# Kernel tuning notes

Hardware: AMD Instinct MI355X
Metric: run time of the kernel (lower is better)

The kernel has to match this reference:

```python
import math
import jax, jax.numpy as jnp
import numpy as np

L = 16
T = 2 ** 19
F = 2
N_MIN = 16
N_MAX = 512
BOUND = 3.0
BATCH = 524288

_b = math.exp((math.log(N_MAX) - math.log(N_MIN)) / (L - 1))
NS = np.array([int(N_MIN * _b ** i) for i in range(L)], dtype=np.float32)  # resolutions per level
PRIMES = np.array([1, 2654435761, 805459861], dtype=np.uint32)
# 8 cube-corner offsets (x,y,z) in {0,1}
OFFSETS = np.array([[x, y, z] for x in (0, 1) for y in (0, 1) for z in (0, 1)], dtype=np.uint32)


def setup_inputs() -> dict:
    key = jax.random.key(0)
    k_pos, k_tab = jax.random.split(key)
    inputs = jax.random.uniform(k_pos, (BATCH, 3), dtype=jnp.float32, minval=-BOUND, maxval=BOUND)
    hash_table = jax.random.uniform(k_tab, (L, T, F), dtype=jnp.float32) * 0.0002 - 0.0001
    return {"inputs": inputs, "hash_table": hash_table}


def reference(inputs, hash_table):
    x = (inputs + BOUND) / (2 * BOUND)                      # [B,3] in [0,1]
    widths = jnp.asarray(1.0 / NS)[:, None, None]           # [L,1,1], width = 1/n per level
    pmin = jnp.floor(x[None] / widths)                      # [L,B,3] floor cell coord (== torch //)
    per = (x[None] - pmin * widths) / widths                # [L,B,3] fractional position in cell
    offs = jnp.asarray(OFFSETS)                             # [8,3] uint32
    corners = pmin.astype(jnp.uint32)[:, :, None, :] + offs[None, None]  # [L,B,8,3]
    prod = corners * jnp.asarray(PRIMES)                    # uint32 mul wraps mod 2^32
    idx = (prod[..., 0] ^ prod[..., 1] ^ prod[..., 2]) % jnp.uint32(T)   # [L,B,8]
    feats = jax.vmap(lambda tab, i: tab[i])(hash_table, idx)             # [L,B,8,F] gathers
    # trilinear weights: use per where offset bit is 1, (1-per) where 0
    w = jnp.prod(jnp.where(offs[None, None].astype(bool), per[:, :, None, :], 1.0 - per[:, :, None, :]), axis=-1)  # [L,B,8]
    feat = jnp.einsum('lbcf,lbc->lbf', feats, w)            # [L,B,F]
    B = inputs.shape[0]
    return feat.transpose(1, 0, 2).reshape(B, L * F)
```

## Files before the change

kernel.cpp:

```cpp
#include <hip/hip_runtime.h>
#include <cstdint>
#include <cstddef>


#define NUM_LEVELS 16
#define TBL_MASK ((1u << 19) - 1u)
#define PRIME_Y 2654435761u
#define PRIME_Z 805459861u
#define BATCH 524288

typedef float nfloat4 __attribute__((ext_vector_type(4)));
typedef double ndouble2 __attribute__((ext_vector_type(2)));

__constant__ float c_ns[NUM_LEVELS] = {
    16.f, 20.f, 25.f, 32.f, 40.f, 50.f, 64.f, 80.f,
    101.f, 128.f, 161.f, 203.f, 256.f, 322.f, 406.f, 512.f
};

__device__ __forceinline__ float2 d2f2(double d) {
    union { double d; float2 f; } u;
    u.d = d;
    return u.f;
}

__device__ __forceinline__ double f22d(float2 f) {
    union { double d; float2 f; } u;
    u.f = f;
    return u.d;
}

__global__ __launch_bounds__(256) void enc_level_kernel(
    const float* __restrict__ in,
    const float* __restrict__ table,
    double* __restrict__ ws,
    int base_level)
{
    const int slot = blockIdx.x & 7;
    const int chunk = blockIdx.x >> 3;
    const int l = base_level + slot;
    const int p = chunk * 256 + threadIdx.x;

    const float vx = __builtin_nontemporal_load(&in[p * 3 + 0]);
    const float vy = __builtin_nontemporal_load(&in[p * 3 + 1]);
    const float vz = __builtin_nontemporal_load(&in[p * 3 + 2]);
    const float xs = (vx + 3.0f) / 6.0f;
    const float ys = (vy + 3.0f) / 6.0f;
    const float zs = (vz + 3.0f) / 6.0f;

    const float n = c_ns[l];
    const float tx = xs * n, ty = ys * n, tz = zs * n;
    const float fpx = floorf(tx), fpy = floorf(ty), fpz = floorf(tz);
    const float wx1 = tx - fpx, wy1 = ty - fpy, wz1 = tz - fpz;
    const uint32_t px = (uint32_t)fpx;
    const uint32_t py = (uint32_t)fpy;
    const uint32_t pz = (uint32_t)fpz;

    const uint32_t hy0 = py * PRIME_Y, hy1 = hy0 + PRIME_Y;
    const uint32_t hz0 = pz * PRIME_Z, hz1 = hz0 + PRIME_Z;
    const uint32_t b0 = hy0 ^ hz0, b1 = hy0 ^ hz1;
    const uint32_t b2 = hy1 ^ hz0, b3 = hy1 ^ hz1;

    const uint32_t i00 = (px ^ b0) & TBL_MASK;
    const uint32_t i01 = (px ^ b1) & TBL_MASK;
    const uint32_t i02 = (px ^ b2) & TBL_MASK;
    const uint32_t i03 = (px ^ b3) & TBL_MASK;
    const uint32_t qx = px + 1u;
    const uint32_t i40 = (qx ^ b0) & TBL_MASK;
    const uint32_t i41 = (qx ^ b1) & TBL_MASK;
    const uint32_t i42 = (qx ^ b2) & TBL_MASK;
    const uint32_t i43 = (qx ^ b3) & TBL_MASK;

    const double* __restrict__ tb = ((const double*)table) + ((size_t)l << 19);
    const ndouble2* __restrict__ tb2 = (const ndouble2*)tb;

    const ndouble2 q0 = tb2[i00 >> 1];
    const ndouble2 q1 = tb2[i01 >> 1];
    const ndouble2 q2 = tb2[i02 >> 1];
    const ndouble2 q3 = tb2[i03 >> 1];

    const bool odd = (px & 1u) != 0u;
    double g0 = 0.0, g1 = 0.0, g2 = 0.0, g3 = 0.0;
    if (odd) {
        g0 = tb[i40];
        g1 = tb[i41];
        g2 = tb[i42];
        g3 = tb[i43];
    }

    const double e00 = (i00 & 1u) ? q0.y : q0.x;
    const double e01 = (i01 & 1u) ? q1.y : q1.x;
    const double e02 = (i02 & 1u) ? q2.y : q2.x;
    const double e03 = (i03 & 1u) ? q3.y : q3.x;
    const double p00 = (i00 & 1u) ? q0.x : q0.y;
    const double p01 = (i01 & 1u) ? q1.x : q1.y;
    const double p02 = (i02 & 1u) ? q2.x : q2.y;
    const double p03 = (i03 & 1u) ? q3.x : q3.y;

    float2 f[8];
    f[0] = d2f2(e00); f[1] = d2f2(e01); f[2] = d2f2(e02); f[3] = d2f2(e03);
    f[4] = d2f2(odd ? g0 : p00);
    f[5] = d2f2(odd ? g1 : p01);
    f[6] = d2f2(odd ? g2 : p02);
    f[7] = d2f2(odd ? g3 : p03);

    const float wx0 = 1.0f - wx1;
    const float wy0 = 1.0f - wy1;
    const float wz0 = 1.0f - wz1;

    float a0 = 0.0f, a1 = 0.0f, w;
    w = wx0 * wy0 * wz0; a0 = fmaf(f[0].x, w, a0); a1 = fmaf(f[0].y, w, a1);
    w = wx0 * wy0 * wz1; a0 = fmaf(f[1].x, w, a0); a1 = fmaf(f[1].y, w, a1);
    w = wx0 * wy1 * wz0; a0 = fmaf(f[2].x, w, a0); a1 = fmaf(f[2].y, w, a1);
    w = wx0 * wy1 * wz1; a0 = fmaf(f[3].x, w, a0); a1 = fmaf(f[3].y, w, a1);
    w = wx1 * wy0 * wz0; a0 = fmaf(f[4].x, w, a0); a1 = fmaf(f[4].y, w, a1);
    w = wx1 * wy0 * wz1; a0 = fmaf(f[5].x, w, a0); a1 = fmaf(f[5].y, w, a1);
    w = wx1 * wy1 * wz0; a0 = fmaf(f[6].x, w, a0); a1 = fmaf(f[6].y, w, a1);
    w = wx1 * wy1 * wz1; a0 = fmaf(f[7].x, w, a0); a1 = fmaf(f[7].y, w, a1);

    __builtin_nontemporal_store(f22d(make_float2(a0, a1)),
                                &ws[(size_t)l * BATCH + p]);
}

__global__ __launch_bounds__(256) void transpose_kernel(
    const double* __restrict__ ws,
    nfloat4* __restrict__ out)
{
    __shared__ double lds[256][NUM_LEVELS + 1];

    const int tid = threadIdx.x;
    const int p0 = blockIdx.x * 256;

#pragma unroll
    for (int l = 0; l < NUM_LEVELS; ++l) {
        lds[tid][l] = __builtin_nontemporal_load(&ws[(size_t)l * BATCH + p0 + tid]);
    }
    __syncthreads();

#pragma unroll
    for (int it = 0; it < 8; ++it) {
        const int e = it * 256 + tid;
        const int p = e >> 3;
        const int j = e & 7;
        const float2 a = d2f2(lds[p][2 * j]);
        const float2 b = d2f2(lds[p][2 * j + 1]);
        nfloat4 r;
        r.x = a.x; r.y = a.y; r.z = b.x; r.w = b.y;
        __builtin_nontemporal_store(r, &out[(size_t)blockIdx.x * 2048 + e]);
    }
}

struct Corner8 {
    uint32_t i[8];
    float wx0, wy0, wz0;
};

__device__ __forceinline__ Corner8 corner_setup_xyz(
    float xs, float ys, float zs, float n)
{
    const float tx = xs * n, ty = ys * n, tz = zs * n;
    const float fpx = floorf(tx), fpy = floorf(ty), fpz = floorf(tz);

    Corner8 c;
    c.wx0 = tx - fpx;
    c.wy0 = ty - fpy;
    c.wz0 = tz - fpz;

    const uint32_t px = (uint32_t)fpx;
    const uint32_t py = (uint32_t)fpy;
    const uint32_t pz = (uint32_t)fpz;

    const uint32_t hx0 = px;
    const uint32_t hx1 = px + 1u;
    const uint32_t hy0 = py * PRIME_Y;
    const uint32_t hy1 = hy0 + PRIME_Y;
    const uint32_t hz0 = pz * PRIME_Z;
    const uint32_t hz1 = hz0 + PRIME_Z;

    c.i[0] = (hx0 ^ hy0 ^ hz0) & TBL_MASK;
    c.i[1] = (hx0 ^ hy0 ^ hz1) & TBL_MASK;
    c.i[2] = (hx0 ^ hy1 ^ hz0) & TBL_MASK;
    c.i[3] = (hx0 ^ hy1 ^ hz1) & TBL_MASK;
    c.i[4] = (hx1 ^ hy0 ^ hz0) & TBL_MASK;
    c.i[5] = (hx1 ^ hy0 ^ hz1) & TBL_MASK;
    c.i[6] = (hx1 ^ hy1 ^ hz0) & TBL_MASK;
    c.i[7] = (hx1 ^ hy1 ^ hz1) & TBL_MASK;
    return c;
}

__device__ __forceinline__ float2 blend8(const Corner8& c, const float2 f[8])
{
    const float wx1 = c.wx0, wx0 = 1.0f - c.wx0;
    const float wy1 = c.wy0, wy0 = 1.0f - c.wy0;
    const float wz1 = c.wz0, wz0 = 1.0f - c.wz0;

    float a0 = 0.0f, a1 = 0.0f, w;
    w = wx0 * wy0 * wz0; a0 = fmaf(f[0].x, w, a0); a1 = fmaf(f[0].y, w, a1);
    w = wx0 * wy0 * wz1; a0 = fmaf(f[1].x, w, a0); a1 = fmaf(f[1].y, w, a1);
    w = wx0 * wy1 * wz0; a0 = fmaf(f[2].x, w, a0); a1 = fmaf(f[2].y, w, a1);
    w = wx0 * wy1 * wz1; a0 = fmaf(f[3].x, w, a0); a1 = fmaf(f[3].y, w, a1);
    w = wx1 * wy0 * wz0; a0 = fmaf(f[4].x, w, a0); a1 = fmaf(f[4].y, w, a1);
    w = wx1 * wy0 * wz1; a0 = fmaf(f[5].x, w, a0); a1 = fmaf(f[5].y, w, a1);
    w = wx1 * wy1 * wz0; a0 = fmaf(f[6].x, w, a0); a1 = fmaf(f[6].y, w, a1);
    w = wx1 * wy1 * wz1; a0 = fmaf(f[7].x, w, a0); a1 = fmaf(f[7].y, w, a1);
    return make_float2(a0, a1);
}

__global__ __launch_bounds__(256) void enc_scatter_kernel(
    const float* __restrict__ in,
    const float* __restrict__ table,
    float2* __restrict__ out)
{
    const int v = blockIdx.x & 15;
    const int chunk = blockIdx.x >> 4;
    const int l = (v < 8) ? (15 - v) : (v - 8);
    const int p = chunk * 256 + threadIdx.x;

    const float vx = in[p * 3 + 0];
    const float vy = in[p * 3 + 1];
    const float vz = in[p * 3 + 2];
    const Corner8 c = corner_setup_xyz((vx + 3.0f) / 6.0f, (vy + 3.0f) / 6.0f,
                                       (vz + 3.0f) / 6.0f, c_ns[l]);
    const double* __restrict__ tb = ((const double*)table) + ((size_t)l << 19);
    float2 f[8];
#pragma unroll
    for (int k = 0; k < 8; ++k) f[k] = d2f2(tb[c.i[k]]);
    out[(size_t)p * NUM_LEVELS + l] = blend8(c, f);
}

extern "C" void kernel_launch(void* const* d_in, const int* in_sizes, int n_in,
                              void* d_out, int out_size, void* d_ws, size_t ws_size,
                              hipStream_t stream) {
    const float* inputs = (const float*)d_in[0];
    const float* table  = (const float*)d_in[1];

    const size_t ws_needed = (size_t)NUM_LEVELS * BATCH * sizeof(float2);

    if (ws_size >= ws_needed) {
        double* ws = (double*)d_ws;
        enc_level_kernel<<<16384, 256, 0, stream>>>(inputs, table, ws, 8);
        enc_level_kernel<<<16384, 256, 0, stream>>>(inputs, table, ws, 0);
        transpose_kernel<<<2048, 256, 0, stream>>>(ws, (nfloat4*)d_out);
    } else {
        enc_scatter_kernel<<<32768, 256, 0, stream>>>(inputs, table, (float2*)d_out);
    }
}
```

Measured before the change: 351.4 us.

## Cache coarse-level dense grids in LDS and tile workspace per chunk

Levels 0 and 1 (resolutions 16 and 20) get their own kernel, which first gathers the full dense 18^3 or 22^3 grid of hashed table entries into LDS. Each point then reads its 8 corners from LDS instead of doing random global gathers. The workspace layout moves from level-major to chunk-major with 256-point tiles, so the transpose kernel reads one contiguous 32KB block per chunk. Level scheduling is also remapped so the 8 concurrent blocks cover contiguous runs within a level. The costs are an extra launch, LDS pressure (about 85KB per block for level 1) and a grid-fill step repeated in each of 128 blocks per level.

```diff
diff --git a/kernel.cpp b/kernel.cpp
--- a/kernel.cpp
+++ b/kernel.cpp
@@ -29,16 +29,22 @@
     return u.d;
 }
 
-__global__ __launch_bounds__(256) void enc_level_kernel(
+__device__ __forceinline__ size_t ws_idx(int p, int l) {
+    return ((size_t)(p >> 8) * NUM_LEVELS + l) * 256 + (p & 255);
+}
+
+__global__ __launch_bounds__(256) void enc_sched_kernel(
     const float* __restrict__ in,
     const float* __restrict__ table,
     double* __restrict__ ws,
-    int base_level)
+    int base_level, int cps)
 {
     const int slot = blockIdx.x & 7;
-    const int chunk = blockIdx.x >> 3;
-    const int l = base_level + slot;
-    const int p = chunk * 256 + threadIdx.x;
+    const int seq  = blockIdx.x >> 3;
+    const int g = slot * cps + seq;
+    const int l = base_level + (g >> 11);
+    const int cil = g & 2047;
+    const int p = cil * 256 + threadIdx.x;
 
     const float vx = __builtin_nontemporal_load(&in[p * 3 + 0]);
     const float vy = __builtin_nontemporal_load(&in[p * 3 + 1]);
@@ -117,8 +123,85 @@
     w = wx1 * wy1 * wz0; a0 = fmaf(f[6].x, w, a0); a1 = fmaf(f[6].y, w, a1);
     w = wx1 * wy1 * wz1; a0 = fmaf(f[7].x, w, a0); a1 = fmaf(f[7].y, w, a1);
 
-    __builtin_nontemporal_store(f22d(make_float2(a0, a1)),
-                                &ws[(size_t)l * BATCH + p]);
+    __builtin_nontemporal_store(f22d(make_float2(a0, a1)), &ws[ws_idx(p, l)]);
+}
+
+template <int LVL, int D>
+__device__ __forceinline__ void coarse_body(
+    const float* __restrict__ in,
+    const float* __restrict__ table,
+    double* __restrict__ ws,
+    double* __restrict__ cache,
+    int part)
+{
+    const int tid = threadIdx.x;
+    const double* __restrict__ tb =
+        ((const double*)table) + ((size_t)LVL << 19);
+
+    for (int c = tid; c < D * D * D; c += 1024) {
+        const uint32_t cz = (uint32_t)(c % D);
+        const uint32_t r  = (uint32_t)(c / D);
+        const uint32_t cy = r % D;
+        const uint32_t cx = r / D;
+        const uint32_t h = (cx ^ (cy * PRIME_Y) ^ (cz * PRIME_Z)) & TBL_MASK;
+        cache[c] = tb[h];
+    }
+    __syncthreads();
+
+    const float n = c_ns[LVL];
+#pragma unroll
+    for (int it = 0; it < 4; ++it) {
+        const int p = part * 4096 + it * 1024 + tid;
+        const float vx = __builtin_nontemporal_load(&in[p * 3 + 0]);
+        const float vy = __builtin_nontemporal_load(&in[p * 3 + 1]);
+        const float vz = __builtin_nontemporal_load(&in[p * 3 + 2]);
+        const float xs = (vx + 3.0f) / 6.0f;
+        const float ys = (vy + 3.0f) / 6.0f;
+        const float zs = (vz + 3.0f) / 6.0f;
+        const float tx = xs * n, ty = ys * n, tz = zs * n;
+        const float fpx = floorf(tx), fpy = floorf(ty), fpz = floorf(tz);
+        const float wx1 = tx - fpx, wy1 = ty - fpy, wz1 = tz - fpz;
+        const int px = (int)fpx, py = (int)fpy, pz = (int)fpz;
+
+        const int base = (px * D + py) * D + pz;
+        float2 f[8];
+        f[0] = d2f2(cache[base]);
+        f[1] = d2f2(cache[base + 1]);
+        f[2] = d2f2(cache[base + D]);
+        f[3] = d2f2(cache[base + D + 1]);
+        f[4] = d2f2(cache[base + D * D]);
+        f[5] = d2f2(cache[base + D * D + 1]);
+        f[6] = d2f2(cache[base + D * D + D]);
+        f[7] = d2f2(cache[base + D * D + D + 1]);
+
+        const float wx0 = 1.0f - wx1;
+        const float wy0 = 1.0f - wy1;
+        const float wz0 = 1.0f - wz1;
+
+        float a0 = 0.0f, a1 = 0.0f, w;
+        w = wx0 * wy0 * wz0; a0 = fmaf(f[0].x, w, a0); a1 = fmaf(f[0].y, w, a1);
+        w = wx0 * wy0 * wz1; a0 = fmaf(f[1].x, w, a0); a1 = fmaf(f[1].y, w, a1);
+        w = wx0 * wy1 * wz0; a0 = fmaf(f[2].x, w, a0); a1 = fmaf(f[2].y, w, a1);
+        w = wx0 * wy1 * wz1; a0 = fmaf(f[3].x, w, a0); a1 = fmaf(f[3].y, w, a1);
+        w = wx1 * wy0 * wz0; a0 = fmaf(f[4].x, w, a0); a1 = fmaf(f[4].y, w, a1);
+        w = wx1 * wy0 * wz1; a0 = fmaf(f[5].x, w, a0); a1 = fmaf(f[5].y, w, a1);
+        w = wx1 * wy1 * wz0; a0 = fmaf(f[6].x, w, a0); a1 = fmaf(f[6].y, w, a1);
+        w = wx1 * wy1 * wz1; a0 = fmaf(f[7].x, w, a0); a1 = fmaf(f[7].y, w, a1);
+
+        __builtin_nontemporal_store(f22d(make_float2(a0, a1)),
+                                    &ws[ws_idx(p, LVL)]);
+    }
+}
+
+__global__ __launch_bounds__(1024) void coarse_kernel(
+    const float* __restrict__ in,
+    const float* __restrict__ table,
+    double* __restrict__ ws)
+{
+    extern __shared__ double cache[];
+    const int part = blockIdx.x & 127;
+    if ((blockIdx.x >> 7) == 0) coarse_body<0, 18>(in, table, ws, cache, part);
+    else                        coarse_body<1, 22>(in, table, ws, cache, part);
 }
 
 __global__ __launch_bounds__(256) void transpose_kernel(
@@ -128,11 +211,11 @@
     __shared__ double lds[256][NUM_LEVELS + 1];
 
     const int tid = threadIdx.x;
-    const int p0 = blockIdx.x * 256;
+    const size_t base = (size_t)blockIdx.x * (NUM_LEVELS * 256);
 
 #pragma unroll
     for (int l = 0; l < NUM_LEVELS; ++l) {
-        lds[tid][l] = __builtin_nontemporal_load(&ws[(size_t)l * BATCH + p0 + tid]);
+        lds[tid][l] = ws[base + (size_t)l * 256 + tid];
     }
     __syncthreads();
 
@@ -237,8 +320,10 @@
 
     if (ws_size >= ws_needed) {
         double* ws = (double*)d_ws;
-        enc_level_kernel<<<16384, 256, 0, stream>>>(inputs, table, ws, 8);
-        enc_level_kernel<<<16384, 256, 0, stream>>>(inputs, table, ws, 0);
+        enc_sched_kernel<<<16384, 256, 0, stream>>>(inputs, table, ws, 8, 2048);
+        enc_sched_kernel<<<12288, 256, 0, stream>>>(inputs, table, ws, 2, 1536);
+        coarse_kernel<<<256, 1024, 22 * 22 * 22 * sizeof(double), stream>>>(
+            inputs, table, ws);
         transpose_kernel<<<2048, 256, 0, stream>>>(ws, (nfloat4*)d_out);
     } else {
         enc_scatter_kernel<<<32768, 256, 0, stream>>>(inputs, table, (float2*)d_out);
```

New measurement: 349.2 us. No clear change (-0.6%).

## Fuse per-level encoding and transpose into single per-point kernel

Applied to the files above, without the earlier changes.

Replaces the two level-split encoding launches, the workspace round-trip and the LDS transpose with one kernel in which each thread loops over all 16 levels for its point. It writes each level pair directly as a float4 into the output, removing the 64 MB workspace write and read and two extra launches. In exchange, each block now touches all 16 hash tables instead of 8, which lowers L2 locality for the gathers. Only 2048 blocks run a serial, non-unrolled level loop, so less memory-level parallelism is exposed. The output stores are also strided per thread rather than coalesced.

```diff
diff --git a/kernel.cpp b/kernel.cpp
--- a/kernel.cpp
+++ b/kernel.cpp
@@ -23,30 +23,10 @@
     return u.f;
 }
 
-__device__ __forceinline__ double f22d(float2 f) {
-    union { double d; float2 f; } u;
-    u.f = f;
-    return u.d;
-}
-
-__global__ __launch_bounds__(256) void enc_level_kernel(
-    const float* __restrict__ in,
-    const float* __restrict__ table,
-    double* __restrict__ ws,
-    int base_level)
+__device__ __forceinline__ float2 level_eval(
+    int l, float xs, float ys, float zs,
+    const double* __restrict__ table_d)
 {
-    const int slot = blockIdx.x & 7;
-    const int chunk = blockIdx.x >> 3;
-    const int l = base_level + slot;
-    const int p = chunk * 256 + threadIdx.x;
-
-    const float vx = __builtin_nontemporal_load(&in[p * 3 + 0]);
-    const float vy = __builtin_nontemporal_load(&in[p * 3 + 1]);
-    const float vz = __builtin_nontemporal_load(&in[p * 3 + 2]);
-    const float xs = (vx + 3.0f) / 6.0f;
-    const float ys = (vy + 3.0f) / 6.0f;
-    const float zs = (vz + 3.0f) / 6.0f;
-
     const float n = c_ns[l];
     const float tx = xs * n, ty = ys * n, tz = zs * n;
     const float fpx = floorf(tx), fpy = floorf(ty), fpz = floorf(tz);
@@ -70,7 +50,7 @@
     const uint32_t i42 = (qx ^ b2) & TBL_MASK;
     const uint32_t i43 = (qx ^ b3) & TBL_MASK;
 
-    const double* __restrict__ tb = ((const double*)table) + ((size_t)l << 19);
+    const double* __restrict__ tb = table_d + ((size_t)l << 19);
     const ndouble2* __restrict__ tb2 = (const ndouble2*)tb;
 
     const ndouble2 q0 = tb2[i00 >> 1];
@@ -116,115 +96,34 @@
     w = wx1 * wy0 * wz1; a0 = fmaf(f[5].x, w, a0); a1 = fmaf(f[5].y, w, a1);
     w = wx1 * wy1 * wz0; a0 = fmaf(f[6].x, w, a0); a1 = fmaf(f[6].y, w, a1);
     w = wx1 * wy1 * wz1; a0 = fmaf(f[7].x, w, a0); a1 = fmaf(f[7].y, w, a1);
-
-    __builtin_nontemporal_store(f22d(make_float2(a0, a1)),
-                                &ws[(size_t)l * BATCH + p]);
-}
-
-__global__ __launch_bounds__(256) void transpose_kernel(
-    const double* __restrict__ ws,
-    nfloat4* __restrict__ out)
-{
-    __shared__ double lds[256][NUM_LEVELS + 1];
-
-    const int tid = threadIdx.x;
-    const int p0 = blockIdx.x * 256;
-
-#pragma unroll
-    for (int l = 0; l < NUM_LEVELS; ++l) {
-        lds[tid][l] = __builtin_nontemporal_load(&ws[(size_t)l * BATCH + p0 + tid]);
-    }
-    __syncthreads();
-
-#pragma unroll
-    for (int it = 0; it < 8; ++it) {
-        const int e = it * 256 + tid;
-        const int p = e >> 3;
-        const int j = e & 7;
-        const float2 a = d2f2(lds[p][2 * j]);
-        const float2 b = d2f2(lds[p][2 * j + 1]);
-        nfloat4 r;
-        r.x = a.x; r.y = a.y; r.z = b.x; r.w = b.y;
-        __builtin_nontemporal_store(r, &out[(size_t)blockIdx.x * 2048 + e]);
-    }
-}
-
-struct Corner8 {
-    uint32_t i[8];
-    float wx0, wy0, wz0;
-};
-
-__device__ __forceinline__ Corner8 corner_setup_xyz(
-    float xs, float ys, float zs, float n)
-{
-    const float tx = xs * n, ty = ys * n, tz = zs * n;
-    const float fpx = floorf(tx), fpy = floorf(ty), fpz = floorf(tz);
-
-    Corner8 c;
-    c.wx0 = tx - fpx;
-    c.wy0 = ty - fpy;
-    c.wz0 = tz - fpz;
-
-    const uint32_t px = (uint32_t)fpx;
-    const uint32_t py = (uint32_t)fpy;
-    const uint32_t pz = (uint32_t)fpz;
-
-    const uint32_t hx0 = px;
-    const uint32_t hx1 = px + 1u;
-    const uint32_t hy0 = py * PRIME_Y;
-    const uint32_t hy1 = hy0 + PRIME_Y;
-    const uint32_t hz0 = pz * PRIME_Z;
-    const uint32_t hz1 = hz0 + PRIME_Z;
-
-    c.i[0] = (hx0 ^ hy0 ^ hz0) & TBL_MASK;
-    c.i[1] = (hx0 ^ hy0 ^ hz1) & TBL_MASK;
-    c.i[2] = (hx0 ^ hy1 ^ hz0) & TBL_MASK;
-    c.i[3] = (hx0 ^ hy1 ^ hz1) & TBL_MASK;
-    c.i[4] = (hx1 ^ hy0 ^ hz0) & TBL_MASK;
-    c.i[5] = (hx1 ^ hy0 ^ hz1) & TBL_MASK;
-    c.i[6] = (hx1 ^ hy1 ^ hz0) & TBL_MASK;
-    c.i[7] = (hx1 ^ hy1 ^ hz1) & TBL_MASK;
-    return c;
-}
-
-__device__ __forceinline__ float2 blend8(const Corner8& c, const float2 f[8])
-{
-    const float wx1 = c.wx0, wx0 = 1.0f - c.wx0;
-    const float wy1 = c.wy0, wy0 = 1.0f - c.wy0;
-    const float wz1 = c.wz0, wz0 = 1.0f - c.wz0;
-
-    float a0 = 0.0f, a1 = 0.0f, w;
-    w = wx0 * wy0 * wz0; a0 = fmaf(f[0].x, w, a0); a1 = fmaf(f[0].y, w, a1);
-    w = wx0 * wy0 * wz1; a0 = fmaf(f[1].x, w, a0); a1 = fmaf(f[1].y, w, a1);
-    w = wx0 * wy1 * wz0; a0 = fmaf(f[2].x, w, a0); a1 = fmaf(f[2].y, w, a1);
-    w = wx0 * wy1 * wz1; a0 = fmaf(f[3].x, w, a0); a1 = fmaf(f[3].y, w, a1);
-    w = wx1 * wy0 * wz0; a0 = fmaf(f[4].x, w, a0); a1 = fmaf(f[4].y, w, a1);
-    w = wx1 * wy0 * wz1; a0 = fmaf(f[5].x, w, a0); a1 = fmaf(f[5].y, w, a1);
-    w = wx1 * wy1 * wz0; a0 = fmaf(f[6].x, w, a0); a1 = fmaf(f[6].y, w, a1);
-    w = wx1 * wy1 * wz1; a0 = fmaf(f[7].x, w, a0); a1 = fmaf(f[7].y, w, a1);
     return make_float2(a0, a1);
 }
 
-__global__ __launch_bounds__(256) void enc_scatter_kernel(
+__global__ __launch_bounds__(256) void enc_fused_kernel(
     const float* __restrict__ in,
     const float* __restrict__ table,
-    float2* __restrict__ out)
+    nfloat4* __restrict__ out)
 {
-    const int v = blockIdx.x & 15;
-    const int chunk = blockIdx.x >> 4;
-    const int l = (v < 8) ? (15 - v) : (v - 8);
-    const int p = chunk * 256 + threadIdx.x;
+    const int p = blockIdx.x * 256 + threadIdx.x;
 
-    const float vx = in[p * 3 + 0];
-    const float vy = in[p * 3 + 1];
-    const float vz = in[p * 3 + 2];
-    const Corner8 c = corner_setup_xyz((vx + 3.0f) / 6.0f, (vy + 3.0f) / 6.0f,
-                                       (vz + 3.0f) / 6.0f, c_ns[l]);
-    const double* __restrict__ tb = ((const double*)table) + ((size_t)l << 19);
-    float2 f[8];
-#pragma unroll
-    for (int k = 0; k < 8; ++k) f[k] = d2f2(tb[c.i[k]]);
-    out[(size_t)p * NUM_LEVELS + l] = blend8(c, f);
+    const float vx = __builtin_nontemporal_load(&in[p * 3 + 0]);
+    const float vy = __builtin_nontemporal_load(&in[p * 3 + 1]);
+    const float vz = __builtin_nontemporal_load(&in[p * 3 + 2]);
+    const float xs = (vx + 3.0f) / 6.0f;
+    const float ys = (vy + 3.0f) / 6.0f;
+    const float zs = (vz + 3.0f) / 6.0f;
+
+    const double* __restrict__ table_d = (const double*)table;
+    nfloat4* __restrict__ op = out + (size_t)p * 8;
+
+#pragma unroll 1
+    for (int lp = 0; lp < 8; ++lp) {
+        const float2 r0 = level_eval(2 * lp + 0, xs, ys, zs, table_d);
+        const float2 r1 = level_eval(2 * lp + 1, xs, ys, zs, table_d);
+        nfloat4 r;
+        r.x = r0.x; r.y = r0.y; r.z = r1.x; r.w = r1.y;
+        op[lp] = r;
+    }
 }
 
 extern "C" void kernel_launch(void* const* d_in, const int* in_sizes, int n_in,
@@ -233,14 +132,5 @@
     const float* inputs = (const float*)d_in[0];
     const float* table  = (const float*)d_in[1];
 
-    const size_t ws_needed = (size_t)NUM_LEVELS * BATCH * sizeof(float2);
-
-    if (ws_size >= ws_needed) {
-        double* ws = (double*)d_ws;
-        enc_level_kernel<<<16384, 256, 0, stream>>>(inputs, table, ws, 8);
-        enc_level_kernel<<<16384, 256, 0, stream>>>(inputs, table, ws, 0);
-        transpose_kernel<<<2048, 256, 0, stream>>>(ws, (nfloat4*)d_out);
-    } else {
-        enc_scatter_kernel<<<32768, 256, 0, stream>>>(inputs, table, (float2*)d_out);
-    }
+    enc_fused_kernel<<<2048, 256, 0, stream>>>(inputs, table, (nfloat4*)d_out);
 }
```

New measurement: 430.4 us. 1.22x slower.
